# Kernel optimization log

Measured on AMD Instinct MI355X. Metric: run time of the kernel, lower is better.

Reference implementation:

```python
import jax, jax.numpy as jnp
import numpy as np

BREAKING_TOKENS = jnp.array([13], dtype=jnp.int64)
NUM_HEADS = 16

B, S, E = 2, 2048, 1024


def setup_inputs() -> dict:
    key = jax.random.key(0)
    k1, k2, k3, k4, k5, k6 = jax.random.split(key, 6)
    scale = 1.0 / np.sqrt(E)
    return {
        "input_embeddings": jax.random.normal(k1, (B, S, E), dtype=jnp.float32),
        "token_ids": jax.random.randint(k2, (B, S), 0, 100, dtype=jnp.int64),
        "in_proj_weight": jax.random.normal(k3, (3 * E, E), dtype=jnp.float32) * scale,
        "in_proj_bias": jax.random.normal(k4, (3 * E,), dtype=jnp.float32) * 0.02,
        "out_proj_weight": jax.random.normal(k5, (E, E), dtype=jnp.float32) * scale,
        "out_proj_bias": jax.random.normal(k6, (E,), dtype=jnp.float32) * 0.02,
    }


def _sentence_mask(token_ids):
    # Faithful vectorization of the triple Python loop:
    # mask[b, i, j] is True iff j <= i and no breaking token occurs at positions j..i.
    brk = jnp.isin(token_ids, BREAKING_TOKENS)            # [B, S] bool
    s = jnp.cumsum(brk.astype(jnp.int32), axis=-1)        # inclusive cumsum of breaks
    s_prev = s - brk.astype(jnp.int32)                    # cumsum up to j-1
    seq = token_ids.shape[-1]
    causal = jnp.tril(jnp.ones((seq, seq), dtype=bool))   # j <= i
    # no break in [j, i]  <=>  s[i] == s_prev[j]
    return causal[None, :, :] & (s[:, :, None] == s_prev[:, None, :])  # [B, S, S]


def reference(input_embeddings, token_ids, in_proj_weight, in_proj_bias,
              out_proj_weight, out_proj_bias):
    x = input_embeddings
    b, s, e = x.shape
    h = NUM_HEADS
    d = e // h

    # torch bool attn_mask semantics: True = NOT allowed to attend (-inf).
    mask_true = _sentence_mask(token_ids)                 # [B, S, S]

    qkv = x @ in_proj_weight.T + in_proj_bias             # [B, S, 3E]
    q, k, v = jnp.split(qkv, 3, axis=-1)
    q = q.reshape(b, s, h, d)
    k = k.reshape(b, s, h, d)
    v = v.reshape(b, s, h, d)

    scores = jnp.einsum("bqhd,bkhd->bhqk", q, k) / jnp.sqrt(jnp.asarray(d, x.dtype))
    scores = jnp.where(mask_true[:, None, :, :], -jnp.inf, scores)
    attn = jax.nn.softmax(scores, axis=-1)                # [B, H, S, S]

    out = jnp.einsum("bhqk,bkhd->bqhd", attn, v).reshape(b, s, e)
    return out @ out_proj_weight.T + out_proj_bias
```

## Files before the change

kernel.cpp:

```cpp
#include <hip/hip_runtime.h>
#include <math.h>
#include <stdint.h>

#define BB 2
#define SS 2048
#define EE 1024
#define HH 16
#define DD 64
#define E3 3072
#define NR (BB*SS)

#define C2Q 0.18033688011112042f

typedef __attribute__((ext_vector_type(8))) short short8;
typedef __attribute__((ext_vector_type(4))) float f32x4;
typedef __attribute__((ext_vector_type(4))) uint uint4v;

__device__ __forceinline__ ushort f2bf(float f) {
    uint u = __float_as_uint(f);
    uint r = u + 0x7FFFu + ((u >> 16) & 1u);
    return (ushort)(r >> 16);
}
__device__ __forceinline__ short8 pack8(float4 a, float4 b) {
    short8 v;
    v[0] = (short)f2bf(a.x); v[1] = (short)f2bf(a.y); v[2] = (short)f2bf(a.z); v[3] = (short)f2bf(a.w);
    v[4] = (short)f2bf(b.x); v[5] = (short)f2bf(b.y); v[6] = (short)f2bf(b.z); v[7] = (short)f2bf(b.w);
    return v;
}
__device__ __forceinline__ uint cvtpk(float lo, float hi) {
    uint d;
    asm("v_cvt_pk_bf16_f32 %0, %1, %2" : "=v"(d) : "v"(lo), "v"(hi));
    return d;
}
__device__ __forceinline__ float vexp2(float x) {
    float r;
    asm("v_exp_f32 %0, %1" : "=v"(r) : "v"(x));
    return r;
}

__global__ __launch_bounds__(256) void cvt_bf16(const float* __restrict__ in,
                                                ushort* __restrict__ out, int n8) {
    int i = blockIdx.x * 256 + threadIdx.x;
    if (i < n8) {
        const float4* p = (const float4*)in + (size_t)i * 2;
        float4 a = p[0], b = p[1];
        *((short8*)out + i) = pack8(a, b);
    }
}

__global__ void scan_kernel(const int* __restrict__ tok, int* __restrict__ lbrk) {
    int b = blockIdx.x;
    int t = threadIdx.x;
    __shared__ int pmax[256];
    int loc[8];
    int base = b * SS + t * 8;
    int lm = -1;
#pragma unroll
    for (int i = 0; i < 8; i++) {
        if (tok[base + i] == 13) lm = t * 8 + i;
        loc[i] = lm;
    }
    pmax[t] = lm;
    __syncthreads();
    if (t == 0) {
        int acc = -1;
        for (int i = 0; i < 256; i++) { int tmp = pmax[i]; pmax[i] = acc; acc = max(acc, tmp); }
    }
    __syncthreads();
    int off = pmax[t];
#pragma unroll
    for (int i = 0; i < 8; i++)
        lbrk[base + i] = max(off, loc[i]);
}

template<int OUT_BF16>
__global__ __launch_bounds__(256) void gemm_mfma(const ushort* __restrict__ A,
                                                 const ushort* __restrict__ Bw,
                                                 const float* __restrict__ bias,
                                                 void* __restrict__ Cv,
                                                 int M, int K) {
    __shared__ ushort As[2][128 * 32];
    __shared__ ushort Bs[2][128 * 32];
    const int bm = blockIdx.x * 128;
    const int bn = blockIdx.y * 128;
    const int tid = threadIdx.x;
    const int w = tid >> 6, lane = tid & 63;
    const int l16 = lane & 15, lk = lane >> 4;
    const int wr = w >> 1, wc = w & 1;

    f32x4 acc[4][4];
#pragma unroll
    for (int mi = 0; mi < 4; mi++)
#pragma unroll
        for (int ni = 0; ni < 4; ni++)
            acc[mi][ni] = (f32x4){0.f, 0.f, 0.f, 0.f};

    const int ci  = w * 2;
    const int rA0 = lane >> 2;
    const int gsh = (lane & 3) ^ ((lane >> 2) & 3);

#define GSTAGE(buf, k0)                                                                      \
    {                                                                                        \
        _Pragma("unroll") for (int i2 = 0; i2 < 2; ++i2) {                                   \
            int c = ci + i2;                                                                 \
            int r = c * 16 + rA0;                                                            \
            const ushort* ga = A + (size_t)(bn + r) * K + (k0) + gsh * 8;                    \
            const ushort* gb = Bw + (size_t)(bm + r) * K + (k0) + gsh * 8;                   \
            __builtin_amdgcn_global_load_lds(                                                \
                (const __attribute__((address_space(1))) void*)ga,                           \
                (__attribute__((address_space(3))) void*)((char*)&As[buf][0] + c * 1024),    \
                16, 0, 0);                                                                   \
            __builtin_amdgcn_global_load_lds(                                                \
                (const __attribute__((address_space(1))) void*)gb,                           \
                (__attribute__((address_space(3))) void*)((char*)&Bs[buf][0] + c * 1024),    \
                16, 0, 0);                                                                   \
        }                                                                                    \
    }

    const int pp = (lk ^ (l16 & 3)) * 8;
    const int NT = K / 32;

    GSTAGE(0, 0);
    __syncthreads();

    for (int t = 0; t < NT; ++t) {
        int cur = t & 1;
        if (t + 1 < NT) GSTAGE(cur ^ 1, (t + 1) * 32);
        const ushort* Ab = &As[cur][0];
        const ushort* Bb = &Bs[cur][0];
        short8 af[4], bfr[4];
#pragma unroll
        for (int mi = 0; mi < 4; ++mi) {
            int r = wr * 64 + mi * 16 + l16;
            af[mi] = *(const short8*)(Ab + r * 32 + pp);
        }
#pragma unroll
        for (int ni = 0; ni < 4; ++ni) {
            int r = wc * 64 + ni * 16 + l16;
            bfr[ni] = *(const short8*)(Bb + r * 32 + pp);
        }
#pragma unroll
        for (int mi = 0; mi < 4; ++mi)
#pragma unroll
            for (int ni = 0; ni < 4; ++ni)
                acc[mi][ni] = __builtin_amdgcn_mfma_f32_16x16x32_bf16(af[mi], bfr[ni], acc[mi][ni], 0, 0, 0);
        __syncthreads();
    }
#undef GSTAGE

#pragma unroll
    for (int ni = 0; ni < 4; ++ni) {
        int col = bm + wc * 64 + ni * 16 + l16;
        float bv = bias[col];
#pragma unroll
        for (int mi = 0; mi < 4; ++mi) {
            int row = bn + wr * 64 + mi * 16 + lk * 4;
#pragma unroll
            for (int j = 0; j < 4; ++j) {
                float vv = acc[mi][ni][j] + bv;
                if (OUT_BF16 && col < EE) vv *= C2Q;
                if (OUT_BF16)
                    ((ushort*)Cv)[(size_t)(row + j) * M + col] = f2bf(vv);
                else
                    ((float*)Cv)[(size_t)(row + j) * M + col] = vv;
            }
        }
    }
}

__global__ __launch_bounds__(256) void vtrans(const ushort* __restrict__ qkv,
                                              ushort* __restrict__ vT) {
    __shared__ __align__(16) ushort ts[64][72];
    const int bid = blockIdx.x;
    const int jt = bid & 31;
    const int h  = (bid >> 5) & 15;
    const int b  = bid >> 9;
    const int tid = threadIdx.x;
    {
        int j = tid >> 2, cg = tid & 3;
        const ushort* src = qkv + (size_t)(b * SS + jt * 64 + j) * E3 + 2 * EE + h * DD + cg * 16;
        uint4 u0 = ((const uint4*)src)[0];
        uint4 u1 = ((const uint4*)src)[1];
        *(uint4*)&ts[j][cg * 16]     = u0;
        *(uint4*)&ts[j][cg * 16 + 8] = u1;
    }
    __syncthreads();
    {
        int d = tid & 63, cq = tid >> 6;
        ushort vals[16];
#pragma unroll
        for (int cc = 0; cc < 16; ++cc) {
            int c = cq * 16 + cc;
            int t32 = c >> 5, c5 = c & 31;
            int a = c5 >> 3, hi = (c5 >> 2) & 1, i = c5 & 3;
            int j = t32 * 32 + hi * 16 + a * 4 + i;
            vals[cc] = ts[j][d];
        }
        ushort* dst = vT + ((size_t)((b * HH + h) * DD + d)) * SS + jt * 64 + cq * 16;
        uint4 o0, o1;
        o0.x = (uint)vals[0] | ((uint)vals[1] << 16);  o0.y = (uint)vals[2] | ((uint)vals[3] << 16);
        o0.z = (uint)vals[4] | ((uint)vals[5] << 16);  o0.w = (uint)vals[6] | ((uint)vals[7] << 16);
        o1.x = (uint)vals[8] | ((uint)vals[9] << 16);  o1.y = (uint)vals[10] | ((uint)vals[11] << 16);
        o1.z = (uint)vals[12] | ((uint)vals[13] << 16); o1.w = (uint)vals[14] | ((uint)vals[15] << 16);
        *(uint4*)dst       = o0;
        *(uint4*)(dst + 8) = o1;
    }
}

__global__ __launch_bounds__(256, 2) void attn_mfma(const ushort* __restrict__ qkv,
                                                    const ushort* __restrict__ vT,
                                                    const int* __restrict__ lbrk,
                                                    ushort* __restrict__ po,
                                                    float* __restrict__ pl) {
    __shared__ ushort ks[2][64 * 64];
    __shared__ ushort vt[2][64 * 64];

    int bid = (blockIdx.x & 7) * 64 + (blockIdx.x >> 3);
    const int kq = bid & 1;
    const int qb = (bid >> 1) & 7;
    const int h  = (bid >> 4) & 15;
    const int b  = bid >> 8;
    const int q0b = qb * 256;
    const int T0 = kq * 16;
    const int tid = threadIdx.x;
    const int w = tid >> 6, lane = tid & 63;
    const int l16 = lane & 15, lk = lane >> 4;
    const int q0w = q0b + w * 64;

    const ushort* qkv_b = qkv + (size_t)(b * SS) * E3;
    const ushort* vT_bh = vT + ((size_t)(b * HH + h)) * DD * SS;

    short8 qf[4][2];
#pragma unroll
    for (int qg = 0; qg < 4; qg++)
#pragma unroll
        for (int kk = 0; kk < 2; kk++)
            qf[qg][kk] = *(const short8*)(qkv_b + (size_t)(q0w + qg * 16 + l16) * E3 + h * DD + kk * 32 + lk * 8);

    int lb1[4]; uint wid[4];
#pragma unroll
    for (int qg = 0; qg < 4; qg++) {
        int q = q0w + qg * 16 + l16;
        int lb = lbrk[b * SS + q];
        lb1[qg] = lb + 1;
        wid[qg] = (uint)(q - lb);
    }

    const int srow = lane >> 3;
    const int slot = lane & 7;
    const ushort* gK[2];
    const ushort* gV[2];
#pragma unroll
    for (int i = 0; i < 2; i++) {
        int r = w * 16 + i * 8 + srow;
        int sl = (slot ^ (r & 7)) << 3;
        gK[i] = qkv_b + (size_t)r * E3 + EE + h * DD + sl;
        gV[i] = vT_bh + (size_t)r * SS + sl;
    }

#define STAGE(buf, kt)                                                                            \
    {                                                                                             \
        _Pragma("unroll") for (int i = 0; i < 2; ++i) {                                           \
            __builtin_amdgcn_global_load_lds(                                                     \
                (const __attribute__((address_space(1))) void*)(gK[i] + (size_t)(kt) * 64 * E3),  \
                (__attribute__((address_space(3))) void*)((char*)&ks[buf][0] + w * 2048 + i * 1024), \
                16, 0, 0);                                                                        \
            __builtin_amdgcn_global_load_lds(                                                     \
                (const __attribute__((address_space(1))) void*)(gV[i] + (size_t)(kt) * 64),       \
                (__attribute__((address_space(3))) void*)((char*)&vt[buf][0] + w * 2048 + i * 1024), \
                16, 0, 0);                                                                        \
        }                                                                                         \
    }

    const int xr = l16 & 7;
    int perm[2];
#pragma unroll
    for (int u = 0; u < 2; u++) perm[u] = ((u * 4 + lk) ^ xr) << 3;

    short8 ones8;
#pragma unroll
    for (int i = 0; i < 8; i++) ones8[i] = (short)0x3F80;

    f32x4 o[4][4];
    f32x4 l_acc[4];
#pragma unroll
    for (int dg = 0; dg < 4; dg++)
#pragma unroll
        for (int qg = 0; qg < 4; qg++)
            o[dg][qg] = (f32x4){0.f, 0.f, 0.f, 0.f};
#pragma unroll
    for (int qg = 0; qg < 4; qg++) l_acc[qg] = (f32x4){0.f, 0.f, 0.f, 0.f};

    const int tmask = qb * 4 + 3;

    STAGE(0, T0);
    STAGE(1, T0 + 1);

    for (int t = 0; t < 16; ++t) {
        if (t < 15) asm volatile("s_waitcnt vmcnt(4)" ::: "memory");
        else        asm volatile("s_waitcnt vmcnt(0)" ::: "memory");
        __builtin_amdgcn_s_barrier();

        const int T = T0 + t;
        const ushort* kb = &ks[t & 1][0];
        const ushort* vb = &vt[t & 1][0];
        const bool domask = (T <= tmask);

#pragma unroll
        for (int t32 = 0; t32 < 2; ++t32) {
            uint pu[4][4];
#pragma unroll
            for (int hi = 0; hi < 2; ++hi) {
                const int jg = t32 * 2 + hi;
                short8 kf0 = *(const short8*)(kb + (jg * 16 + l16) * 64 + perm[0]);
                short8 kf1 = *(const short8*)(kb + (jg * 16 + l16) * 64 + perm[1]);
                f32x4 s[4];
#pragma unroll
                for (int qg = 0; qg < 4; qg++) {
                    s[qg] = (f32x4){0.f, 0.f, 0.f, 0.f};
                    s[qg] = __builtin_amdgcn_mfma_f32_16x16x32_bf16(kf0, qf[qg][0], s[qg], 0, 0, 0);
                    s[qg] = __builtin_amdgcn_mfma_f32_16x16x32_bf16(kf1, qf[qg][1], s[qg], 0, 0, 0);
                }
                const int jbase = T * 64 + t32 * 32 + hi * 16 + lk * 4;
#pragma unroll
                for (int qg = 0; qg < 4; qg++) {
                    float p0, p1, p2, p3;
                    if (domask) {
                        int jb = jbase - lb1[qg];
                        p0 = vexp2((uint)(jb + 0) < wid[qg] ? -1e30f : s[qg][0]);
                        p1 = vexp2((uint)(jb + 1) < wid[qg] ? -1e30f : s[qg][1]);
                        p2 = vexp2((uint)(jb + 2) < wid[qg] ? -1e30f : s[qg][2]);
                        p3 = vexp2((uint)(jb + 3) < wid[qg] ? -1e30f : s[qg][3]);
                    } else {
                        p0 = vexp2(s[qg][0]);
                        p1 = vexp2(s[qg][1]);
                        p2 = vexp2(s[qg][2]);
                        p3 = vexp2(s[qg][3]);
                    }
                    pu[qg][hi * 2]     = cvtpk(p0, p1);
                    pu[qg][hi * 2 + 1] = cvtpk(p2, p3);
                }
            }
            short8 pfB[4];
#pragma unroll
            for (int qg = 0; qg < 4; qg++) {
                uint4v u;
                u[0] = pu[qg][0]; u[1] = pu[qg][1]; u[2] = pu[qg][2]; u[3] = pu[qg][3];
                pfB[qg] = __builtin_bit_cast(short8, u);
            }
#pragma unroll
            for (int qg = 0; qg < 4; qg++)
                l_acc[qg] = __builtin_amdgcn_mfma_f32_16x16x32_bf16(ones8, pfB[qg], l_acc[qg], 0, 0, 0);
#pragma unroll
            for (int dg = 0; dg < 4; dg++) {
                short8 vf = *(const short8*)(vb + (dg * 16 + l16) * 64 + perm[t32]);
#pragma unroll
                for (int qg = 0; qg < 4; qg++)
                    o[dg][qg] = __builtin_amdgcn_mfma_f32_16x16x32_bf16(vf, pfB[qg], o[dg][qg], 0, 0, 0);
            }
        }

        asm volatile("s_waitcnt lgkmcnt(0)" ::: "memory");
        __builtin_amdgcn_s_barrier();
        if (t + 2 < 16) STAGE(t & 1, T0 + t + 2);
    }
#undef STAGE

    ushort* po_k = po + (size_t)kq * NR * EE;
#pragma unroll
    for (int qg = 0; qg < 4; qg++) {
        int qo = q0w + qg * 16 + l16;
        ushort* dst = po_k + (size_t)(b * SS + qo) * EE + h * DD + lk * 4;
#pragma unroll
        for (int dg = 0; dg < 4; dg++) {
            uint u0 = cvtpk(o[dg][qg][0], o[dg][qg][1]);
            uint u1 = cvtpk(o[dg][qg][2], o[dg][qg][3]);
            uint2 pk; pk.x = u0; pk.y = u1;
            *(uint2*)(dst + dg * 16) = pk;
        }
        if (lk == 0)
            pl[((size_t)(kq * BB + b) * HH + h) * SS + qo] = l_acc[qg][0];
    }
}

__global__ __launch_bounds__(256) void combine(const ushort* __restrict__ po,
                                               const float* __restrict__ pl,
                                               ushort* __restrict__ aob) {
    int i8 = blockIdx.x * 256 + threadIdx.x;
    const int bq = i8 >> 7;
    const int h  = (i8 >> 3) & 15;
    const int b  = bq >> 11;
    const int q  = bq & 2047;
    float l0 = pl[((size_t)(0 * BB + b) * HH + h) * SS + q];
    float l1 = pl[((size_t)(1 * BB + b) * HH + h) * SS + q];
    float inv = 1.f / (l0 + l1);
    short8 a0 = *((const short8*)po + i8);
    short8 a1 = *((const short8*)(po + (size_t)NR * EE) + i8);
    short8 r;
#pragma unroll
    for (int j = 0; j < 8; j++) {
        float f0 = __uint_as_float(((uint)(ushort)a0[j]) << 16);
        float f1 = __uint_as_float(((uint)(ushort)a1[j]) << 16);
        r[j] = (short)f2bf((f0 + f1) * inv);
    }
    *((short8*)aob + i8) = r;
}

extern "C" void kernel_launch(void* const* d_in, const int* in_sizes, int n_in,
                              void* d_out, int out_size, void* d_ws, size_t ws_size,
                              hipStream_t stream) {
    const float* x    = (const float*)d_in[0];
    const int*   tok  = (const int*)d_in[1];
    const float* win  = (const float*)d_in[2];
    const float* bin  = (const float*)d_in[3];
    const float* wout = (const float*)d_in[4];
    const float* bout = (const float*)d_in[5];
    float* out = (float*)d_out;

    ushort* xb    = (ushort*)d_ws;
    ushort* winb  = xb + (size_t)NR * EE;
    ushort* woutb = winb + (size_t)E3 * EE;
    ushort* qkvb  = woutb + (size_t)EE * EE;
    ushort* aob   = qkvb + (size_t)NR * E3;
    ushort* vTb   = aob + (size_t)NR * EE;
    ushort* po    = vTb + (size_t)BB * HH * DD * SS;
    float*  pl    = (float*)(po + (size_t)2 * NR * EE);
    int* lbrk  = (int*)(pl + (size_t)2 * BB * HH * SS);

    int nx8 = NR * EE / 8, nwin8 = E3 * EE / 8, nwout8 = EE * EE / 8;
    cvt_bf16<<<(nx8 + 255) / 256, 256, 0, stream>>>(x, xb, nx8);
    cvt_bf16<<<(nwin8 + 255) / 256, 256, 0, stream>>>(win, winb, nwin8);
    cvt_bf16<<<(nwout8 + 255) / 256, 256, 0, stream>>>(wout, woutb, nwout8);

    scan_kernel<<<BB, 256, 0, stream>>>(tok, lbrk);

    gemm_mfma<1><<<dim3(E3 / 128, NR / 128), 256, 0, stream>>>(xb, winb, bin, (void*)qkvb, E3, EE);

    vtrans<<<BB * HH * (SS / 64), 256, 0, stream>>>(qkvb, vTb);

    attn_mfma<<<BB * HH * (SS / 256) * 2, 256, 0, stream>>>(qkvb, vTb, lbrk, po, pl);

    combine<<<NR * EE / 8 / 256, 256, 0, stream>>>(po, pl, aob);

    gemm_mfma<0><<<dim3(EE / 128, NR / 128), 256, 0, stream>>>(aob, woutb, bout, (void*)out, EE, EE);
}
```

Measured before the change: 139.9 us.

## Fuse V transpose into QKV GEMM epilogue, merge conversions, split KV four ways

The QKV GEMM epilogue now writes V directly in the transposed, permuted layout the attention kernel expects, which removes the separate vtrans kernel and the V columns of the qkv buffer. The three fp32-to-bf16 conversion launches are merged into one kernel. Attention splits the key range into four chunks instead of two, doubling the grid, and the combine kernel sums four partials. Workspace buffers are aliased (po reuses winb, aob reuses xb). The trade-offs are uncoalesced scattered stores in the GEMM epilogue, more partial-output traffic in combine, and the dropped occupancy hint on attn_mfma.

```diff
diff --git a/kernel.cpp b/kernel.cpp
--- a/kernel.cpp
+++ b/kernel.cpp
@@ -9,6 +9,8 @@
 #define DD 64
 #define E3 3072
 #define NR (BB*SS)
+#define QKW 2048
+#define NSPLIT 4
 
 #define C2Q 0.18033688011112042f
 
@@ -38,14 +40,21 @@
     return r;
 }
 
-__global__ __launch_bounds__(256) void cvt_bf16(const float* __restrict__ in,
-                                                ushort* __restrict__ out, int n8) {
+__global__ __launch_bounds__(256) void cvt_all(const float* __restrict__ x,
+                                               const float* __restrict__ win,
+                                               const float* __restrict__ wout,
+                                               ushort* __restrict__ xb,
+                                               ushort* __restrict__ winb,
+                                               ushort* __restrict__ woutb) {
+    const int NX = NR * EE / 8, NW = E3 * EE / 8;
     int i = blockIdx.x * 256 + threadIdx.x;
-    if (i < n8) {
-        const float4* p = (const float4*)in + (size_t)i * 2;
-        float4 a = p[0], b = p[1];
-        *((short8*)out + i) = pack8(a, b);
-    }
+    const float* src; ushort* dst; int j;
+    if (i < NX)           { src = x;    dst = xb;    j = i; }
+    else if (i < NX + NW) { src = win;  dst = winb;  j = i - NX; }
+    else                  { src = wout; dst = woutb; j = i - NX - NW; }
+    const float4* p = (const float4*)src + (size_t)j * 2;
+    float4 a = p[0], b = p[1];
+    *((short8*)dst + j) = pack8(a, b);
 }
 
 __global__ void scan_kernel(const int* __restrict__ tok, int* __restrict__ lbrk) {
@@ -78,7 +87,8 @@
                                                  const ushort* __restrict__ Bw,
                                                  const float* __restrict__ bias,
                                                  void* __restrict__ Cv,
-                                                 int M, int K) {
+                                                 ushort* __restrict__ vTp,
+                                                 int strideC, int K) {
     __shared__ ushort As[2][128 * 32];
     __shared__ ushort Bs[2][128 * 32];
     const int bm = blockIdx.x * 128;
@@ -152,82 +162,56 @@
     for (int ni = 0; ni < 4; ++ni) {
         int col = bm + wc * 64 + ni * 16 + l16;
         float bv = bias[col];
+        const bool isV = OUT_BF16 && (col >= 2 * EE);
 #pragma unroll
         for (int mi = 0; mi < 4; ++mi) {
             int row = bn + wr * 64 + mi * 16 + lk * 4;
-#pragma unroll
-            for (int j = 0; j < 4; ++j) {
-                float vv = acc[mi][ni][j] + bv;
-                if (OUT_BF16 && col < EE) vv *= C2Q;
-                if (OUT_BF16)
-                    ((ushort*)Cv)[(size_t)(row + j) * M + col] = f2bf(vv);
-                else
-                    ((float*)Cv)[(size_t)(row + j) * M + col] = vv;
+            if (isV) {
+                int d   = col - 2 * EE;
+                int bb2 = row >> 11;
+                int tok = row & 2047;
+                int c0  = (tok & ~31) | (lk << 3) | ((mi & 1) << 2);
+                uint2 pk;
+                pk.x = cvtpk(acc[mi][ni][0] + bv, acc[mi][ni][1] + bv);
+                pk.y = cvtpk(acc[mi][ni][2] + bv, acc[mi][ni][3] + bv);
+                *(uint2*)(vTp + ((size_t)(bb2 * HH + (d >> 6)) * DD + (d & 63)) * SS + c0) = pk;
+            } else {
+#pragma unroll
+                for (int j = 0; j < 4; ++j) {
+                    float vv = acc[mi][ni][j] + bv;
+                    if (OUT_BF16 && col < EE) vv *= C2Q;
+                    if (OUT_BF16)
+                        ((ushort*)Cv)[(size_t)(row + j) * strideC + col] = f2bf(vv);
+                    else
+                        ((float*)Cv)[(size_t)(row + j) * strideC + col] = vv;
+                }
             }
         }
     }
 }
 
-__global__ __launch_bounds__(256) void vtrans(const ushort* __restrict__ qkv,
-                                              ushort* __restrict__ vT) {
-    __shared__ __align__(16) ushort ts[64][72];
-    const int bid = blockIdx.x;
-    const int jt = bid & 31;
+__global__ __launch_bounds__(256) void attn_mfma(const ushort* __restrict__ qk,
+                                                 const ushort* __restrict__ vT,
+                                                 const int* __restrict__ lbrk,
+                                                 ushort* __restrict__ po,
+                                                 float* __restrict__ pl) {
+    __shared__ ushort ks[2][64 * 64];
+    __shared__ ushort vt[2][64 * 64];
+
+    int bid = (blockIdx.x & 7) * 128 + (blockIdx.x >> 3);
+    const int kq = bid & 3;
+    const int qb = (bid >> 2) & 7;
     const int h  = (bid >> 5) & 15;
     const int b  = bid >> 9;
-    const int tid = threadIdx.x;
-    {
-        int j = tid >> 2, cg = tid & 3;
-        const ushort* src = qkv + (size_t)(b * SS + jt * 64 + j) * E3 + 2 * EE + h * DD + cg * 16;
-        uint4 u0 = ((const uint4*)src)[0];
-        uint4 u1 = ((const uint4*)src)[1];
-        *(uint4*)&ts[j][cg * 16]     = u0;
-        *(uint4*)&ts[j][cg * 16 + 8] = u1;
-    }
-    __syncthreads();
-    {
-        int d = tid & 63, cq = tid >> 6;
-        ushort vals[16];
-#pragma unroll
-        for (int cc = 0; cc < 16; ++cc) {
-            int c = cq * 16 + cc;
-            int t32 = c >> 5, c5 = c & 31;
-            int a = c5 >> 3, hi = (c5 >> 2) & 1, i = c5 & 3;
-            int j = t32 * 32 + hi * 16 + a * 4 + i;
-            vals[cc] = ts[j][d];
-        }
-        ushort* dst = vT + ((size_t)((b * HH + h) * DD + d)) * SS + jt * 64 + cq * 16;
-        uint4 o0, o1;
-        o0.x = (uint)vals[0] | ((uint)vals[1] << 16);  o0.y = (uint)vals[2] | ((uint)vals[3] << 16);
-        o0.z = (uint)vals[4] | ((uint)vals[5] << 16);  o0.w = (uint)vals[6] | ((uint)vals[7] << 16);
-        o1.x = (uint)vals[8] | ((uint)vals[9] << 16);  o1.y = (uint)vals[10] | ((uint)vals[11] << 16);
-        o1.z = (uint)vals[12] | ((uint)vals[13] << 16); o1.w = (uint)vals[14] | ((uint)vals[15] << 16);
-        *(uint4*)dst       = o0;
-        *(uint4*)(dst + 8) = o1;
-    }
-}
-
-__global__ __launch_bounds__(256, 2) void attn_mfma(const ushort* __restrict__ qkv,
-                                                    const ushort* __restrict__ vT,
-                                                    const int* __restrict__ lbrk,
-                                                    ushort* __restrict__ po,
-                                                    float* __restrict__ pl) {
-    __shared__ ushort ks[2][64 * 64];
-    __shared__ ushort vt[2][64 * 64];
-
-    int bid = (blockIdx.x & 7) * 64 + (blockIdx.x >> 3);
-    const int kq = bid & 1;
-    const int qb = (bid >> 1) & 7;
-    const int h  = (bid >> 4) & 15;
-    const int b  = bid >> 8;
     const int q0b = qb * 256;
-    const int T0 = kq * 16;
+    const int T0 = kq * 8;
+    const int NTT = 8;
     const int tid = threadIdx.x;
     const int w = tid >> 6, lane = tid & 63;
     const int l16 = lane & 15, lk = lane >> 4;
     const int q0w = q0b + w * 64;
 
-    const ushort* qkv_b = qkv + (size_t)(b * SS) * E3;
+    const ushort* qk_b  = qk + (size_t)(b * SS) * QKW;
     const ushort* vT_bh = vT + ((size_t)(b * HH + h)) * DD * SS;
 
     short8 qf[4][2];
@@ -235,7 +219,7 @@
     for (int qg = 0; qg < 4; qg++)
 #pragma unroll
         for (int kk = 0; kk < 2; kk++)
-            qf[qg][kk] = *(const short8*)(qkv_b + (size_t)(q0w + qg * 16 + l16) * E3 + h * DD + kk * 32 + lk * 8);
+            qf[qg][kk] = *(const short8*)(qk_b + (size_t)(q0w + qg * 16 + l16) * QKW + h * DD + kk * 32 + lk * 8);
 
     int lb1[4]; uint wid[4];
 #pragma unroll
@@ -254,7 +238,7 @@
     for (int i = 0; i < 2; i++) {
         int r = w * 16 + i * 8 + srow;
         int sl = (slot ^ (r & 7)) << 3;
-        gK[i] = qkv_b + (size_t)r * E3 + EE + h * DD + sl;
+        gK[i] = qk_b + (size_t)r * QKW + EE + h * DD + sl;
         gV[i] = vT_bh + (size_t)r * SS + sl;
     }
 
@@ -262,7 +246,7 @@
     {                                                                                             \
         _Pragma("unroll") for (int i = 0; i < 2; ++i) {                                           \
             __builtin_amdgcn_global_load_lds(                                                     \
-                (const __attribute__((address_space(1))) void*)(gK[i] + (size_t)(kt) * 64 * E3),  \
+                (const __attribute__((address_space(1))) void*)(gK[i] + (size_t)(kt) * 64 * QKW), \
                 (__attribute__((address_space(3))) void*)((char*)&ks[buf][0] + w * 2048 + i * 1024), \
                 16, 0, 0);                                                                        \
             __builtin_amdgcn_global_load_lds(                                                     \
@@ -296,9 +280,9 @@
     STAGE(0, T0);
     STAGE(1, T0 + 1);
 
-    for (int t = 0; t < 16; ++t) {
-        if (t < 15) asm volatile("s_waitcnt vmcnt(4)" ::: "memory");
-        else        asm volatile("s_waitcnt vmcnt(0)" ::: "memory");
+    for (int t = 0; t < NTT; ++t) {
+        if (t < NTT - 1) asm volatile("s_waitcnt vmcnt(4)" ::: "memory");
+        else             asm volatile("s_waitcnt vmcnt(0)" ::: "memory");
         __builtin_amdgcn_s_barrier();
 
         const int T = T0 + t;
@@ -362,7 +346,7 @@
 
         asm volatile("s_waitcnt lgkmcnt(0)" ::: "memory");
         __builtin_amdgcn_s_barrier();
-        if (t + 2 < 16) STAGE(t & 1, T0 + t + 2);
+        if (t + 2 < NTT) STAGE(t & 1, T0 + t + 2);
     }
 #undef STAGE
 
@@ -391,18 +375,23 @@
     const int h  = (i8 >> 3) & 15;
     const int b  = bq >> 11;
     const int q  = bq & 2047;
-    float l0 = pl[((size_t)(0 * BB + b) * HH + h) * SS + q];
-    float l1 = pl[((size_t)(1 * BB + b) * HH + h) * SS + q];
-    float inv = 1.f / (l0 + l1);
-    short8 a0 = *((const short8*)po + i8);
-    short8 a1 = *((const short8*)(po + (size_t)NR * EE) + i8);
+    float lsum = 0.f;
+#pragma unroll
+    for (int k = 0; k < NSPLIT; k++)
+        lsum += pl[((size_t)(k * BB + b) * HH + h) * SS + q];
+    float inv = 1.f / lsum;
+    float accv[8] = {0.f};
+#pragma unroll
+    for (int k = 0; k < NSPLIT; k++) {
+        short8 a = *((const short8*)(po + (size_t)k * NR * EE) + i8);
+#pragma unroll
+        for (int j = 0; j < 8; j++)
+            accv[j] += __uint_as_float(((uint)(ushort)a[j]) << 16);
+    }
     short8 r;
 #pragma unroll
-    for (int j = 0; j < 8; j++) {
-        float f0 = __uint_as_float(((uint)(ushort)a0[j]) << 16);
-        float f1 = __uint_as_float(((uint)(ushort)a1[j]) << 16);
-        r[j] = (short)f2bf((f0 + f1) * inv);
-    }
+    for (int j = 0; j < 8; j++)
+        r[j] = (short)f2bf(accv[j] * inv);
     *((short8*)aob + i8) = r;
 }
 
@@ -418,29 +407,25 @@
     float* out = (float*)d_out;
 
     ushort* xb    = (ushort*)d_ws;
-    ushort* winb  = xb + (size_t)NR * EE;
-    ushort* woutb = winb + (size_t)E3 * EE;
-    ushort* qkvb  = woutb + (size_t)EE * EE;
-    ushort* aob   = qkvb + (size_t)NR * E3;
-    ushort* vTb   = aob + (size_t)NR * EE;
-    ushort* po    = vTb + (size_t)BB * HH * DD * SS;
-    float*  pl    = (float*)(po + (size_t)2 * NR * EE);
-    int* lbrk  = (int*)(pl + (size_t)2 * BB * HH * SS);
-
-    int nx8 = NR * EE / 8, nwin8 = E3 * EE / 8, nwout8 = EE * EE / 8;
-    cvt_bf16<<<(nx8 + 255) / 256, 256, 0, stream>>>(x, xb, nx8);
-    cvt_bf16<<<(nwin8 + 255) / 256, 256, 0, stream>>>(win, winb, nwin8);
-    cvt_bf16<<<(nwout8 + 255) / 256, 256, 0, stream>>>(wout, woutb, nwout8);
+    ushort* woutb = xb + (size_t)NR * EE;
+    ushort* qkb   = woutb + (size_t)EE * EE;
+    ushort* vTb   = qkb + (size_t)NR * QKW;
+    float*  pl    = (float*)(vTb + (size_t)BB * HH * DD * SS);
+    int*    lbrk  = (int*)(pl + (size_t)NSPLIT * BB * HH * SS);
+    ushort* winb  = (ushort*)(lbrk + NR);
+    ushort* po    = winb;
+    ushort* aob   = xb;
+
+    int ncvt = (NR * EE + E3 * EE + EE * EE) / 8;
+    cvt_all<<<ncvt / 256, 256, 0, stream>>>(x, win, wout, xb, winb, woutb);
 
     scan_kernel<<<BB, 256, 0, stream>>>(tok, lbrk);
 
-    gemm_mfma<1><<<dim3(E3 / 128, NR / 128), 256, 0, stream>>>(xb, winb, bin, (void*)qkvb, E3, EE);
-
-    vtrans<<<BB * HH * (SS / 64), 256, 0, stream>>>(qkvb, vTb);
-
-    attn_mfma<<<BB * HH * (SS / 256) * 2, 256, 0, stream>>>(qkvb, vTb, lbrk, po, pl);
+    gemm_mfma<1><<<dim3(E3 / 128, NR / 128), 256, 0, stream>>>(xb, winb, bin, (void*)qkb, vTb, QKW, EE);
+
+    attn_mfma<<<BB * HH * (SS / 256) * NSPLIT, 256, 0, stream>>>(qkb, vTb, lbrk, po, pl);
 
     combine<<<NR * EE / 8 / 256, 256, 0, stream>>>(po, pl, aob);
 
-    gemm_mfma<0><<<dim3(EE / 128, NR / 128), 256, 0, stream>>>(aob, woutb, bout, (void*)out, EE, EE);
-}
+    gemm_mfma<0><<<dim3(EE / 128, NR / 128), 256, 0, stream>>>(aob, woutb, bout, (void*)out, nullptr, EE, EE);
+}
```

Result: slower. 175.8 us (+25.6%).
